# Performance work log

Hardware: AMD Instinct MI355X
Metric: run time of the kernel (lower is better)

Reference implementation:

```python
import jax, jax.numpy as jnp
import numpy as np

B, S, D, H, HD = 2, 2048, 1024, 16, 64


def setup_inputs() -> dict:
    key = jax.random.key(0)
    ks = jax.random.split(key, 11)
    scale_in = 1.0 / np.sqrt(D)
    return {
        "query": jax.random.normal(ks[0], (B, S, D), jnp.float32),
        "key": jax.random.normal(ks[1], (B, S, D), jnp.float32),
        "value": jax.random.normal(ks[2], (B, S, D), jnp.float32),
        "Wq": jax.random.normal(ks[3], (H, D, HD), jnp.float32) * scale_in,
        "bq": jax.random.normal(ks[4], (H, HD), jnp.float32) * 0.02,
        "Wk": jax.random.normal(ks[5], (H, D, HD), jnp.float32) * scale_in,
        "bk": jax.random.normal(ks[6], (H, HD), jnp.float32) * 0.02,
        "Wv": jax.random.normal(ks[7], (H, D, HD), jnp.float32) * scale_in,
        "bv": jax.random.normal(ks[8], (H, HD), jnp.float32) * 0.02,
        "Wo": jax.random.normal(ks[9], (D, D), jnp.float32) * scale_in,
        "bo": jax.random.normal(ks[10], (D,), jnp.float32) * 0.02,
    }


def reference(query, key, value, Wq, bq, Wk, bk, Wv, bv, Wo, bo):
    # Per-head projections, batched over heads (equivalent to the ModuleList loop).
    q = jnp.einsum('bsd,hdk->bhsk', query, Wq) + bq[None, :, None, :]   # [B,H,S,HD]
    k = jnp.einsum('bsd,hdk->bhsk', key, Wk) + bk[None, :, None, :]
    v = jnp.einsum('bsd,hdk->bhsk', value, Wv) + bv[None, :, None, :]
    scale = 1.0 / jnp.sqrt(jnp.asarray(q.shape[-1], q.dtype))
    scores = jnp.einsum('bhsk,bhtk->bhst', q, k) * scale                # [B,H,S,S]
    attn = jax.nn.softmax(scores, axis=-1)
    ctx = jnp.einsum('bhst,bhtk->bhsk', attn, v)                        # [B,H,S,HD]
    # Concat heads along last dim: [B,S,H*HD] == [B,S,D]
    x = jnp.transpose(ctx, (0, 2, 1, 3)).reshape(ctx.shape[0], ctx.shape[2], -1)
    return x @ Wo + bo
```

## Files before the change

### kernel.cpp

```cpp
#include <hip/hip_runtime.h>
#include <hip/hip_bf16.h>

typedef __bf16 bf16;
typedef __bf16 bf16x8 __attribute__((ext_vector_type(8)));
typedef __bf16 bf16x4 __attribute__((ext_vector_type(4)));
typedef __bf16 bf16x2 __attribute__((ext_vector_type(2)));
typedef float floatx4 __attribute__((ext_vector_type(4)));
typedef float floatx16 __attribute__((ext_vector_type(16)));
typedef int intx4 __attribute__((ext_vector_type(4)));

#define B_SZ 2
#define S_LEN 2048
#define D_DIM 1024
#define H_CNT 16
#define HD_DIM 64
#define M_ROWS 4096
#define QSCALE 0.18033688011112042f

__device__ __forceinline__ void async_ld16(const bf16* g, bf16* s) {
    __builtin_amdgcn_global_load_lds((const __attribute__((address_space(1))) void*)g,
                                     (__attribute__((address_space(3))) void*)s, 16, 0, 0);
}

__device__ __forceinline__ floatx4 mfma16(bf16x8 a, bf16x8 b, floatx4 c) {
    return __builtin_amdgcn_mfma_f32_16x16x32_bf16(a, b, c, 0, 0, 0);
}
__device__ __forceinline__ floatx16 mfma32(bf16x8 a, bf16x8 b, floatx16 c) {
    return __builtin_amdgcn_mfma_f32_32x32x16_bf16(a, b, c, 0, 0, 0);
}

__device__ __forceinline__ bf16x8 mkfrag(int a0, int a1, int b0, int b1) {
    asm("v_permlane32_swap_b32 %0, %1" : "+v"(a0), "+v"(b0));
    asm("v_permlane32_swap_b32 %0, %1" : "+v"(a1), "+v"(b1));
    intx4 q = {a0, a1, b0, b1};
    return __builtin_bit_cast(bf16x8, q);
}

struct PrepArgs {
    const float* cast_src[3]; bf16* cast_dst[3];
    const float* w_src[3];    bf16* w_dst[3];
    const float* wo;          bf16* wo_t;
};
__global__ __launch_bounds__(256) void prep(PrepArgs a) {
    __shared__ bf16 tile[32][33];
    const int bx = blockIdx.x, tid = threadIdx.x;
    if (bx < 12288) {
        const int t = bx >> 12, blk = bx & 4095;
        const float* s = a.cast_src[t];
        bf16* d = a.cast_dst[t];
        size_t i = ((size_t)blk * 256 + tid) * 4;
        float4 v = *(const float4*)(s + i);
        bf16x4 o = { (bf16)v.x, (bf16)v.y, (bf16)v.z, (bf16)v.w };
        *(bf16x4*)(d + i) = o;
        return;
    }
    int tx = tid & 31, ty = tid >> 5;
    const float* src; bf16* dst; int r0, c0, C, R;
    if (bx < 15360) {
        int idx = bx - 12288;
        int z = idx >> 6, xy = idx & 63;
        int mat = z >> 4, head = z & 15;
        src = a.w_src[mat] + (size_t)head * D_DIM * HD_DIM;
        dst = a.w_dst[mat] + (size_t)head * D_DIM * HD_DIM;
        r0 = (xy & 31) * 32; c0 = (xy >> 5) * 32; C = HD_DIM; R = D_DIM;
    } else {
        int idx = bx - 15360;
        src = a.wo; dst = a.wo_t;
        r0 = (idx & 31) * 32; c0 = (idx >> 5) * 32; C = D_DIM; R = D_DIM;
    }
#pragma unroll
    for (int i = 0; i < 32; i += 8)
        tile[ty + i][tx] = (bf16)src[(size_t)(r0 + ty + i) * C + c0 + tx];
    __syncthreads();
#pragma unroll
    for (int i = 0; i < 32; i += 8)
        dst[(size_t)(c0 + ty + i) * R + r0 + tx] = tile[tx][ty + i];
}

struct GemmPtrs { const bf16* A; const bf16* BT; const float* bias; bf16* C; float* Cf;
                  float scale; int mode; };
struct GemmArgs { GemmPtrs p[3]; };

__global__ __launch_bounds__(256) void gemm_bt(GemmArgs args) {
    __shared__ __align__(16) bf16 As[128 * 32];
    __shared__ __align__(16) bf16 Bs[128 * 32];
    const GemmPtrs P = args.p[blockIdx.z];
    const int tid = threadIdx.x, wave = tid >> 6, lane = tid & 63;
    const int quad = lane >> 4, l15 = lane & 15;
    const int bm = blockIdx.x * 128, bn = blockIdx.y * 128;
    const int wm = (wave >> 1) * 64, wn = (wave & 1) * 64;

    floatx4 acc[4][4];
#pragma unroll
    for (int i = 0; i < 4; i++)
#pragma unroll
        for (int j = 0; j < 4; j++) acc[i][j] = (floatx4){0.f, 0.f, 0.f, 0.f};

    const int srow = (lane >> 2);
    const int scol = (((lane & 3) ^ ((srow >> 1) & 3)) << 3);
    const int ck = ((quad ^ ((l15 >> 1) & 3)) << 3);
    for (int k0 = 0; k0 < 1024; k0 += 32) {
#pragma unroll
        for (int it = 0; it < 2; ++it) {
            int issue = it * 4 + wave;
            int row = issue * 16 + srow;
            async_ld16(P.A + (size_t)(bm + row) * 1024 + k0 + scol, &As[issue * 512]);
            async_ld16(P.BT + (size_t)(bn + row) * 1024 + k0 + scol, &Bs[issue * 512]);
        }
        __syncthreads();
        bf16x8 af[4], bfr[4];
#pragma unroll
        for (int mi = 0; mi < 4; mi++)
            af[mi] = *(const bf16x8*)&As[(wm + mi * 16 + l15) * 32 + ck];
#pragma unroll
        for (int ni = 0; ni < 4; ni++)
            bfr[ni] = *(const bf16x8*)&Bs[(wn + ni * 16 + l15) * 32 + ck];
#pragma unroll
        for (int mi = 0; mi < 4; mi++)
#pragma unroll
            for (int ni = 0; ni < 4; ni++) acc[mi][ni] = mfma16(af[mi], bfr[ni], acc[mi][ni]);
        __syncthreads();
    }
#pragma unroll
    for (int ni = 0; ni < 4; ni++) {
        int col = bn + wn + ni * 16 + l15;
        float bb = P.bias[col];
#pragma unroll
        for (int mi = 0; mi < 4; mi++) {
#pragma unroll
            for (int r = 0; r < 4; r++) {
                int row = bm + wm + mi * 16 + quad * 4 + r;
                float v = (acc[mi][ni][r] + bb) * P.scale;
                if (P.mode == 0) {
                    P.Cf[(size_t)row * 1024 + col] = v;
                } else {
                    int b = row >> 11, s2 = row & 2047, h = col >> 6, hd = col & 63;
                    if (P.mode == 1)
                        P.C[(((size_t)(b * H_CNT + h)) * S_LEN + s2) * HD_DIM + hd] = (bf16)v;
                    else
                        P.C[(((size_t)(b * H_CNT + h)) * HD_DIM + hd) * S_LEN + s2] = (bf16)v;
                }
            }
        }
    }
}

__global__ __launch_bounds__(512, 4) void attn(const bf16* __restrict__ Qg, const bf16* __restrict__ Kg,
                                               const bf16* __restrict__ Vtg, bf16* __restrict__ ctx) {
    __shared__ __align__(16) bf16 smem[32768];
    const int tid = threadIdx.x, wave = tid >> 6, lane = tid & 63;
    const int l31 = lane & 31, half = lane >> 5;
    const int grp = wave >> 2, wg = wave & 3;
    const int bid = blockIdx.x;
    const int bh = (bid >> 1) & 31;
    const int qb = ((bid >> 6) << 1) | (bid & 1);
    const int q0blk = qb * 128;
    const bf16* Kp = Kg + (size_t)bh * S_LEN * HD_DIM;
    const bf16* Vp = Vtg + (size_t)bh * HD_DIM * S_LEN;
    const int tbase = grp * 1024;

    const int f0 = wg * 512 + lane * 8, f1 = (wg + 4) * 512 + lane * 8;
    const int kc0 = f0 >> 9, kt0 = (f0 >> 3) & 63;
    const int kc1 = f1 >> 9, kt1 = (f1 >> 3) & 63;
    bf16* const Kbase = smem + grp * 8192;
    bf16* const Vbase = smem + 16384 + grp * 8192;

#define STAGE(BUF, T0) do { \
        bf16* Kd = Kbase + (BUF) * 4096; \
        bf16* Vd = Vbase + (BUF) * 4096; \
        async_ld16(Kp + (size_t)((T0) + kt0) * HD_DIM + kc0 * 8, Kd + wg * 512); \
        async_ld16(Kp + (size_t)((T0) + kt1) * HD_DIM + kc1 * 8, Kd + (wg + 4) * 512); \
        async_ld16(Vp + (size_t)kt0 * S_LEN + (T0) + kc0 * 8, Vd + wg * 512); \
        async_ld16(Vp + (size_t)kt1 * S_LEN + (T0) + kc1 * 8, Vd + (wg + 4) * 512); \
    } while (0)

    STAGE(0, tbase);
    bf16x8 qf[4];
    {
        const bf16* qrow = Qg + ((size_t)bh * S_LEN + q0blk + wg * 32 + l31) * HD_DIM;
#pragma unroll
        for (int kb = 0; kb < 4; ++kb)
            qf[kb] = *(const bf16x8*)(qrow + (2 * kb + half) * 8);
    }
    __syncthreads();

    float l_i = 0.f;
    floatx16 o0 = {0}, o1 = {0};

    for (int rd = 0; rd < 16; ++rd) {
        const int cur = rd & 1;
        if (rd < 15) STAGE(cur ^ 1, tbase + (rd + 1) * 64);
        const bf16* Kt = Kbase + cur * 4096;
        const bf16* Vt = Vbase + cur * 4096;
        floatx16 sc0 = {0}, sc1 = {0};
        __builtin_amdgcn_s_setprio(1);
#pragma unroll
        for (int kb = 0; kb < 4; ++kb) {
            bf16x8 k0 = *(const bf16x8*)&Kt[(2 * kb + half) * 512 + l31 * 8];
            bf16x8 k1 = *(const bf16x8*)&Kt[(2 * kb + half) * 512 + (32 + l31) * 8];
            sc0 = mfma32(k0, qf[kb], sc0);
            sc1 = mfma32(k1, qf[kb], sc1);
        }
        __builtin_amdgcn_s_setprio(0);
        float rs = 0.f;
        int w0[8], w1[8];
#pragma unroll
        for (int e = 0; e < 16; e += 2) {
            float p0 = __builtin_amdgcn_exp2f(sc0[e]);
            float p1 = __builtin_amdgcn_exp2f(sc0[e + 1]);
            rs += p0 + p1;
            bf16x2 t2 = {(bf16)p0, (bf16)p1};
            w0[e >> 1] = __builtin_bit_cast(int, t2);
        }
#pragma unroll
        for (int e = 0; e < 16; e += 2) {
            float p0 = __builtin_amdgcn_exp2f(sc1[e]);
            float p1 = __builtin_amdgcn_exp2f(sc1[e + 1]);
            rs += p0 + p1;
            bf16x2 t2 = {(bf16)p0, (bf16)p1};
            w1[e >> 1] = __builtin_bit_cast(int, t2);
        }
        l_i += rs;
        bf16x8 pfr[4];
        pfr[0] = mkfrag(w0[0], w0[1], w0[2], w0[3]);
        pfr[1] = mkfrag(w0[4], w0[5], w0[6], w0[7]);
        pfr[2] = mkfrag(w1[0], w1[1], w1[2], w1[3]);
        pfr[3] = mkfrag(w1[4], w1[5], w1[6], w1[7]);
        __builtin_amdgcn_s_setprio(1);
#pragma unroll
        for (int kb = 0; kb < 4; ++kb) {
            bf16x8 v0 = *(const bf16x8*)&Vt[(2 * kb + half) * 512 + l31 * 8];
            bf16x8 v1 = *(const bf16x8*)&Vt[(2 * kb + half) * 512 + (32 + l31) * 8];
            o0 = mfma32(v0, pfr[kb], o0);
            o1 = mfma32(v1, pfr[kb], o1);
        }
        __builtin_amdgcn_s_setprio(0);
        __syncthreads();
    }
#undef STAGE

    l_i += __shfl_xor(l_i, 32);

    float* slabF = (float*)smem;
    float* lA = slabF + 4 * 2112;
    if (grp == 0) {
        float* S0 = slabF + wg * 2112;
#pragma unroll
        for (int s2 = 0; s2 < 2; ++s2) {
            const floatx16 oo = s2 ? o1 : o0;
#pragma unroll
            for (int e = 0; e < 16; ++e) {
                int hd = s2 * 32 + (e & 3) + 8 * (e >> 2) + 4 * half;
                S0[l31 * 66 + hd] = oo[e];
            }
        }
        if (lane < 32) lA[wg * 32 + l31] = l_i;
    }
    __syncthreads();
    if (grp == 1) {
        float* S0 = slabF + wg * 2112;
        float lt = l_i + lA[wg * 32 + l31];
        float inv = 1.f / lt;
        int b = bh >> 4, hh = bh & 15;
        bf16* Sw = smem + 17408 + wg * 1280;
#pragma unroll
        for (int s2 = 0; s2 < 2; ++s2) {
            const floatx16 oo = s2 ? o1 : o0;
#pragma unroll
            for (int e = 0; e < 16; ++e) {
                int hd = (e & 3) + 8 * (e >> 2) + 4 * half;
                float v = (oo[e] + S0[l31 * 66 + s2 * 32 + hd]) * inv;
                Sw[l31 * 40 + hd] = (bf16)v;
            }
#pragma unroll
            for (int p = 0; p < 2; ++p) {
                int q = p * 16 + (lane >> 2), part = lane & 3;
                bf16x8 v = *(const bf16x8*)&Sw[q * 40 + part * 8];
                int s = q0blk + wg * 32 + q;
                *(bf16x8*)&ctx[((size_t)(b * S_LEN + s)) * D_DIM + hh * 64 + s2 * 32 + part * 8] = v;
            }
        }
    }
}

extern "C" void kernel_launch(void* const* d_in, const int* in_sizes, int n_in,
                              void* d_out, int out_size, void* d_ws, size_t ws_size,
                              hipStream_t stream) {
    const float* query = (const float*)d_in[0];
    const float* key   = (const float*)d_in[1];
    const float* value = (const float*)d_in[2];
    const float* Wq = (const float*)d_in[3];
    const float* bq = (const float*)d_in[4];
    const float* Wk = (const float*)d_in[5];
    const float* bk = (const float*)d_in[6];
    const float* Wv = (const float*)d_in[7];
    const float* bv = (const float*)d_in[8];
    const float* Wo = (const float*)d_in[9];
    const float* bo = (const float*)d_in[10];
    float* out = (float*)d_out;

    bf16* ws = (bf16*)d_ws;
    const size_t ASZ = (size_t)M_ROWS * D_DIM;
    const size_t WSZ = (size_t)H_CNT * D_DIM * HD_DIM;
    const size_t TSZ = (size_t)B_SZ * H_CNT * S_LEN * HD_DIM;
    bf16* Qc  = ws;
    bf16* Kc  = Qc + ASZ;
    bf16* Vc  = Kc + ASZ;
    bf16* WqT = Vc + ASZ;
    bf16* WkT = WqT + WSZ;
    bf16* WvT = WkT + WSZ;
    bf16* WoT = WvT + WSZ;
    bf16* Qb  = WoT + (size_t)D_DIM * D_DIM;
    bf16* Kb  = Qb + TSZ;
    bf16* Vtb = Kb + TSZ;
    bf16* ctx = Vtb + TSZ;

    dim3 blk(256);

    PrepArgs pa;
    pa.cast_src[0] = query; pa.cast_src[1] = key; pa.cast_src[2] = value;
    pa.cast_dst[0] = Qc;    pa.cast_dst[1] = Kc;  pa.cast_dst[2] = Vc;
    pa.w_src[0] = Wq; pa.w_src[1] = Wk; pa.w_src[2] = Wv;
    pa.w_dst[0] = WqT; pa.w_dst[1] = WkT; pa.w_dst[2] = WvT;
    pa.wo = Wo; pa.wo_t = WoT;
    prep<<<dim3(16384), blk, 0, stream>>>(pa);

    GemmArgs qkv;
    qkv.p[0] = {Qc, WqT, bq, Qb, nullptr, QSCALE, 1};
    qkv.p[1] = {Kc, WkT, bk, Kb, nullptr, 1.0f, 1};
    qkv.p[2] = {Vc, WvT, bv, Vtb, nullptr, 1.0f, 2};
    gemm_bt<<<dim3(32, 8, 3), blk, 0, stream>>>(qkv);

    attn<<<dim3(512), dim3(512), 0, stream>>>(Qb, Kb, Vtb, ctx);

    GemmArgs og;
    og.p[0] = {ctx, WoT, bo, nullptr, out, 1.0f, 0};
    og.p[1] = og.p[0]; og.p[2] = og.p[0];
    gemm_bt<<<dim3(32, 8, 1), blk, 0, stream>>>(og);
}
```

Baseline: 221.9 us.

## Split attention key range across four wave groups with 1024-thread blocks

```diff
diff --git a/kernel.cpp b/kernel.cpp
--- a/kernel.cpp
+++ b/kernel.cpp
@@ -145,8 +145,8 @@
     }
 }
 
-__global__ __launch_bounds__(512, 4) void attn(const bf16* __restrict__ Qg, const bf16* __restrict__ Kg,
-                                               const bf16* __restrict__ Vtg, bf16* __restrict__ ctx) {
+__global__ __launch_bounds__(1024, 8) void attn(const bf16* __restrict__ Qg, const bf16* __restrict__ Kg,
+                                                const bf16* __restrict__ Vtg, bf16* __restrict__ ctx) {
     __shared__ __align__(16) bf16 smem[32768];
     const int tid = threadIdx.x, wave = tid >> 6, lane = tid & 63;
     const int l31 = lane & 31, half = lane >> 5;
@@ -157,21 +157,17 @@
     const int q0blk = qb * 128;
     const bf16* Kp = Kg + (size_t)bh * S_LEN * HD_DIM;
     const bf16* Vp = Vtg + (size_t)bh * HD_DIM * S_LEN;
-    const int tbase = grp * 1024;
-
-    const int f0 = wg * 512 + lane * 8, f1 = (wg + 4) * 512 + lane * 8;
-    const int kc0 = f0 >> 9, kt0 = (f0 >> 3) & 63;
-    const int kc1 = f1 >> 9, kt1 = (f1 >> 3) & 63;
-    bf16* const Kbase = smem + grp * 8192;
-    bf16* const Vbase = smem + 16384 + grp * 8192;
+    const int tbase = grp * 512;
+
+    const int f = wg * 512 + lane * 8;
+    const int kof = ((f >> 3) & 31) * HD_DIM + (f >> 8) * 8;
+    const int vof = ((f >> 3) & 63) * S_LEN + (f >> 9) * 8;
+    bf16* const Kbase = smem + grp * 4096;
+    bf16* const Vbase = smem + 16384 + grp * 4096;
 
 #define STAGE(BUF, T0) do { \
-        bf16* Kd = Kbase + (BUF) * 4096; \
-        bf16* Vd = Vbase + (BUF) * 4096; \
-        async_ld16(Kp + (size_t)((T0) + kt0) * HD_DIM + kc0 * 8, Kd + wg * 512); \
-        async_ld16(Kp + (size_t)((T0) + kt1) * HD_DIM + kc1 * 8, Kd + (wg + 4) * 512); \
-        async_ld16(Vp + (size_t)kt0 * S_LEN + (T0) + kc0 * 8, Vd + wg * 512); \
-        async_ld16(Vp + (size_t)kt1 * S_LEN + (T0) + kc1 * 8, Vd + (wg + 4) * 512); \
+        async_ld16(Kp + (size_t)(T0) * HD_DIM + kof, Kbase + (BUF) * 2048 + wg * 512); \
+        async_ld16(Vp + (size_t)(T0) + vof,          Vbase + (BUF) * 2048 + wg * 512); \
     } while (0)
 
     STAGE(0, tbase);
@@ -189,21 +185,19 @@
 
     for (int rd = 0; rd < 16; ++rd) {
         const int cur = rd & 1;
-        if (rd < 15) STAGE(cur ^ 1, tbase + (rd + 1) * 64);
-        const bf16* Kt = Kbase + cur * 4096;
-        const bf16* Vt = Vbase + cur * 4096;
-        floatx16 sc0 = {0}, sc1 = {0};
+        if (rd < 15) STAGE(cur ^ 1, tbase + (rd + 1) * 32);
+        const bf16* Kt = Kbase + cur * 2048;
+        const bf16* Vt = Vbase + cur * 2048;
+        floatx16 sc0 = {0};
         __builtin_amdgcn_s_setprio(1);
 #pragma unroll
         for (int kb = 0; kb < 4; ++kb) {
-            bf16x8 k0 = *(const bf16x8*)&Kt[(2 * kb + half) * 512 + l31 * 8];
-            bf16x8 k1 = *(const bf16x8*)&Kt[(2 * kb + half) * 512 + (32 + l31) * 8];
+            bf16x8 k0 = *(const bf16x8*)&Kt[(2 * kb + half) * 256 + l31 * 8];
             sc0 = mfma32(k0, qf[kb], sc0);
-            sc1 = mfma32(k1, qf[kb], sc1);
         }
         __builtin_amdgcn_s_setprio(0);
         float rs = 0.f;
-        int w0[8], w1[8];
+        int w0[8];
 #pragma unroll
         for (int e = 0; e < 16; e += 2) {
             float p0 = __builtin_amdgcn_exp2f(sc0[e]);
@@ -212,27 +206,17 @@
             bf16x2 t2 = {(bf16)p0, (bf16)p1};
             w0[e >> 1] = __builtin_bit_cast(int, t2);
         }
-#pragma unroll
-        for (int e = 0; e < 16; e += 2) {
-            float p0 = __builtin_amdgcn_exp2f(sc1[e]);
-            float p1 = __builtin_amdgcn_exp2f(sc1[e + 1]);
-            rs += p0 + p1;
-            bf16x2 t2 = {(bf16)p0, (bf16)p1};
-            w1[e >> 1] = __builtin_bit_cast(int, t2);
-        }
         l_i += rs;
-        bf16x8 pfr[4];
-        pfr[0] = mkfrag(w0[0], w0[1], w0[2], w0[3]);
-        pfr[1] = mkfrag(w0[4], w0[5], w0[6], w0[7]);
-        pfr[2] = mkfrag(w1[0], w1[1], w1[2], w1[3]);
-        pfr[3] = mkfrag(w1[4], w1[5], w1[6], w1[7]);
+        bf16x8 pfr0 = mkfrag(w0[0], w0[1], w0[2], w0[3]);
+        bf16x8 pfr1 = mkfrag(w0[4], w0[5], w0[6], w0[7]);
         __builtin_amdgcn_s_setprio(1);
 #pragma unroll
-        for (int kb = 0; kb < 4; ++kb) {
+        for (int kb = 0; kb < 2; ++kb) {
             bf16x8 v0 = *(const bf16x8*)&Vt[(2 * kb + half) * 512 + l31 * 8];
             bf16x8 v1 = *(const bf16x8*)&Vt[(2 * kb + half) * 512 + (32 + l31) * 8];
-            o0 = mfma32(v0, pfr[kb], o0);
-            o1 = mfma32(v1, pfr[kb], o1);
+            bf16x8 pf = kb ? pfr1 : pfr0;
+            o0 = mfma32(v0, pf, o0);
+            o1 = mfma32(v1, pf, o1);
         }
         __builtin_amdgcn_s_setprio(0);
         __syncthreads();
@@ -243,8 +227,8 @@
 
     float* slabF = (float*)smem;
     float* lA = slabF + 4 * 2112;
+    float* S0 = slabF + wg * 2112;
     if (grp == 0) {
-        float* S0 = slabF + wg * 2112;
 #pragma unroll
         for (int s2 = 0; s2 < 2; ++s2) {
             const floatx16 oo = s2 ? o1 : o0;
@@ -258,7 +242,32 @@
     }
     __syncthreads();
     if (grp == 1) {
-        float* S0 = slabF + wg * 2112;
+#pragma unroll
+        for (int s2 = 0; s2 < 2; ++s2) {
+            const floatx16 oo = s2 ? o1 : o0;
+#pragma unroll
+            for (int e = 0; e < 16; ++e) {
+                int hd = s2 * 32 + (e & 3) + 8 * (e >> 2) + 4 * half;
+                S0[l31 * 66 + hd] += oo[e];
+            }
+        }
+        if (lane < 32) lA[wg * 32 + l31] += l_i;
+    }
+    __syncthreads();
+    if (grp == 2) {
+#pragma unroll
+        for (int s2 = 0; s2 < 2; ++s2) {
+            const floatx16 oo = s2 ? o1 : o0;
+#pragma unroll
+            for (int e = 0; e < 16; ++e) {
+                int hd = s2 * 32 + (e & 3) + 8 * (e >> 2) + 4 * half;
+                S0[l31 * 66 + hd] += oo[e];
+            }
+        }
+        if (lane < 32) lA[wg * 32 + l31] += l_i;
+    }
+    __syncthreads();
+    if (grp == 3) {
         float lt = l_i + lA[wg * 32 + l31];
         float inv = 1.f / lt;
         int b = bh >> 4, hh = bh & 15;
@@ -331,7 +340,7 @@
     qkv.p[2] = {Vc, WvT, bv, Vtb, nullptr, 1.0f, 2};
     gemm_bt<<<dim3(32, 8, 3), blk, 0, stream>>>(qkv);
 
-    attn<<<dim3(512), dim3(512), 0, stream>>>(Qb, Kb, Vtb, ctx);
+    attn<<<dim3(512), dim3(1024), 0, stream>>>(Qb, Kb, Vtb, ctx);
 
     GemmArgs og;
     og.p[0] = {ctx, WoT, bo, nullptr, out, 1.0f, 0};
```

Result: slower. 445.6 us (+100.8%).
